# Kernel tuning notes

Hardware: AMD Instinct MI355X
Metric: run time of the kernel (lower is better)

Reference implementation:

```python
import jax, jax.numpy as jnp
import numpy as np

B, N, D, H = 128, 512, 128, 8
DK = D // H
CLIP = 10.0                      # tanh_clipping
NORM = float(np.sqrt(D))         # norm_factor = sqrt(embedding_dim), used as multiplier (as in source)


def setup_inputs() -> dict:
    key = jax.random.key(0)
    ks = jax.random.split(key, 7)
    std = float(1.0 / np.sqrt(D))
    return {
        "embeddings": jax.random.normal(ks[0], (B, N, D), dtype=jnp.float32),
        "eval_seq": jax.random.randint(ks[1], (B, N), 0, N, dtype=jnp.int32),
        "W_placeholder": jax.random.uniform(ks[2], (2 * D,), jnp.float32, -std, std),
        "W_node": jax.random.normal(ks[3], (D, 3 * D), jnp.float32) * std,
        "W_fixed": jax.random.normal(ks[4], (D, D), jnp.float32) * std,
        "W_step": jax.random.normal(ks[5], (2 * D, D), jnp.float32) * std,
        "W_out": jax.random.normal(ks[6], (D, D), jnp.float32) * std,
    }


def _decode(embeddings, eval_seq, W_placeholder, W_node, W_fixed, W_step, W_out):
    # Precomputed (fixed) projections, as in the torch module before the decode loop
    proj = embeddings @ W_node                                  # [B,N,3D]
    gK, gV, lK = jnp.split(proj, 3, axis=-1)
    gK = gK.reshape(B, N, H, DK).transpose(2, 0, 1, 3)          # [H,B,N,dk]
    gV = gV.reshape(B, N, H, DK).transpose(2, 0, 1, 3)          # [H,B,N,dk]
    fixed = embeddings.mean(axis=1) @ W_fixed                   # [B,D]
    batch_ix = jnp.arange(B)

    def step_logp(ctx, mask):
        # ctx: [B,2D] step context; mask: [B,N] bool (True = visited)
        query = fixed + ctx @ W_step                            # [B,D]
        qh = query.reshape(B, H, DK)
        compat = NORM * jnp.einsum('bhd,hbnd->hbn', qh, gK)     # [H,B,N]
        compat = jnp.where(mask[None], -jnp.inf, compat)        # mask_inner
        attn = jax.nn.softmax(compat, axis=-1)
        heads = jnp.einsum('hbn,hbnd->hbd', attn, gV)           # [H,B,dk]
        glimpse = heads.transpose(1, 0, 2).reshape(B, D) @ W_out
        logits = NORM * jnp.einsum('bnd,bd->bn', lK, glimpse)   # [B,N]
        logits = jnp.tanh(logits) * CLIP
        logits = jnp.where(mask, -jnp.inf, logits)              # mask_logits
        return jax.nn.log_softmax(logits, axis=-1)              # temp = 1.0

    # step 0: W_placeholder context, empty mask
    mask0 = jnp.zeros((B, N), dtype=bool)
    ctx0 = jnp.broadcast_to(W_placeholder[None, :], (B, 2 * D))
    lp0 = step_logp(ctx0, mask0)
    sel0 = eval_seq[:, 0]
    mask1 = mask0.at[batch_ix, sel0].set(True)
    emb_first = embeddings[batch_ix, sel0]                      # [B,D] (constant across steps)

    def body(carry, sel_i):
        mask, last = carry
        ctx = jnp.concatenate([emb_first, embeddings[batch_ix, last]], axis=-1)  # [B,2D]
        lp = step_logp(ctx, mask)
        new_mask = mask.at[batch_ix, sel_i].set(True)           # update mask AFTER computing log_p
        return (new_mask, sel_i), lp

    (_, _), lps = jax.lax.scan(body, (mask1, sel0), eval_seq[:, 1:].T)  # lps: [N-1,B,N]
    log_p = jnp.concatenate([lp0[None], lps], axis=0).transpose(1, 0, 2)  # [B,N,N]
    return log_p


def reference(embeddings, eval_seq, W_placeholder, W_node, W_fixed, W_step, W_out):
    log_p = _decode(embeddings, eval_seq, W_placeholder, W_node, W_fixed, W_step, W_out)
    return log_p, eval_seq
```

## Files before the change

### kernel.cpp

```cpp
#include <hip/hip_runtime.h>
#include <math.h>

#define B_ 128
#define N_ 512
#define D_ 128
#define H_ 8
#define NORM_ 11.313708498984761f
#define SC_ 16.322324f
#define HSC_ 32.644648f
#define CLIP_ 10.0f
#define MASKC_ -3.0e38f
#define NEG_BIG_ -1.0e30f
#define L2E_ 1.4426950408889634f
#define LN2_ 0.6931471805599453f

typedef unsigned short ushortx;
typedef __attribute__((ext_vector_type(8))) short s8v;
typedef __attribute__((ext_vector_type(4))) float f4v;

#define MFMA_ __builtin_amdgcn_mfma_f32_16x16x32_bf16

__device__ __forceinline__ unsigned short f2bf(float x) {
  union { float f; unsigned u; } v; v.f = x;
  unsigned r = v.u + 0x7fffu + ((v.u >> 16) & 1u);
  return (unsigned short)(r >> 16);
}
__device__ __forceinline__ float bf2f(ushortx u) {
  union { unsigned u; float f; } v; v.u = ((unsigned)u) << 16; return v.f;
}
__device__ __forceinline__ unsigned cvtpk(float lo, float hi) {
  unsigned r;
  asm("v_cvt_pk_bf16_f32 %0, %1, %2" : "=v"(r) : "v"(lo), "v"(hi));
  return r;
}
__device__ __forceinline__ float exp2_hw(float x) {
  float r; asm("v_exp_f32 %0, %1" : "=v"(r) : "v"(x)); return r;
}
__device__ __forceinline__ float log2_hw(float x) {
  float r; asm("v_log_f32 %0, %1" : "=v"(r) : "v"(x)); return r;
}
__device__ __forceinline__ float rcp_hw(float x) {
  float r; asm("v_rcp_f32 %0, %1" : "=v"(r) : "v"(x)); return r;
}
__device__ __forceinline__ float max3f(float a, float b, float c) {
  float r; asm("v_max3_f32 %0, %1, %2, %3" : "=v"(r) : "v"(a), "v"(b), "v"(c));
  return r;
}

__global__ __launch_bounds__(128)
void wfold2(const float* __restrict__ Wnode, const float* __restrict__ Wout,
            const float* __restrict__ Wstep, ushortx* __restrict__ WfT,
            ushortx* __restrict__ WsbT) {
  const int c = blockIdx.x;
  const int k = threadIdx.x;
  if (c < 256) {
    WfT[c * 128 + k] = f2bf(Wnode[k * 384 + c]);
  } else if (c < 384) {
    const int d = c - 256;
    float s = 0.f;
    #pragma unroll 4
    for (int j = 0; j < 128; ++j) s += Wnode[k * 384 + 256 + j] * Wout[d * 128 + j];
    WfT[c * 128 + k] = f2bf(s);
  } else {
    const int d = c - 384;
    WsbT[d * 128 + k] = f2bf(Wstep[(128 + k) * 128 + d] * SC_);
  }
}

__global__ void t_init(int* __restrict__ T) {
  T[blockIdx.x * 256 + threadIdx.x] = 0x7fffffff;
}
__global__ void t_scatter(const int* __restrict__ seq, int* __restrict__ T) {
  const int i = blockIdx.x * 256 + threadIdx.x;
  const int b = i >> 9, st = i & 511;
  atomicMin(&T[b * N_ + seq[i]], st + 1);
}

__global__ __launch_bounds__(512)
void sortperm(const int* __restrict__ seq, const int* __restrict__ T,
              ushortx* __restrict__ K, ushortx* __restrict__ n_orig) {
  const int b = blockIdx.x;
  const int t = threadIdx.x;
  const int lane = t & 63, wv = t >> 6;
  __shared__ int wsum[8];
  __shared__ int tot_s;

  const int node = seq[b * 512 + t];
  const int f = (T[b * 512 + node] == t + 1) ? 1 : 0;
  const unsigned long long bal = __ballot(f);
  const int excl = __popcll(bal & ((1ull << lane) - 1ull));
  if (lane == 0) wsum[wv] = __popcll(bal);
  __syncthreads();
  int woff = 0;
  #pragma unroll
  for (int i = 0; i < 8; ++i) woff += (i < wv) ? wsum[i] : 0;
  const int Kt = woff + excl;
  K[b * 512 + t] = (ushortx)Kt;
  if (f) n_orig[b * 512 + Kt] = (ushortx)node;
  if (t == 511) tot_s = Kt + f;

  const int g = (T[b * 512 + t] == 0x7fffffff) ? 1 : 0;
  const unsigned long long bal2 = __ballot(g);
  const int excl2 = __popcll(bal2 & ((1ull << lane) - 1ull));
  const int w2 = __popcll(bal2);
  __syncthreads();
  if (lane == 0) wsum[wv] = w2;
  __syncthreads();
  int woff2 = 0;
  #pragma unroll
  for (int i = 0; i < 8; ++i) woff2 += (i < wv) ? wsum[i] : 0;
  if (g) n_orig[b * 512 + tot_s + woff2 + excl2] = (ushortx)t;
}

__global__ __launch_bounds__(256)
void proj_mfma(const float* __restrict__ E, const ushortx* __restrict__ WfT,
               const ushortx* __restrict__ n_orig,
               ushortx* __restrict__ gK, ushortx* __restrict__ gVt,
               ushortx* __restrict__ lKt) {
  __shared__ ushortx S[64 * 216];
  const int tid = threadIdx.x;
  const int w = tid >> 6, l = tid & 63;
  const int m16 = l & 15, lg = l >> 4;
  const int b = blockIdx.x >> 3;
  const int n0 = (blockIdx.x & 7) * 64;
  const int p_row = n0 + w * 16 + m16;
  const int orig = (int)n_orig[b * 512 + p_row];
  const float* er = E + ((size_t)b * 512 + orig) * 128;

  s8v af[4];
  #pragma unroll
  for (int ks = 0; ks < 4; ++ks) {
    float4 f0 = *(const float4*)(er + ks * 32 + lg * 8);
    float4 f1 = *(const float4*)(er + ks * 32 + lg * 8 + 4);
    union { unsigned u[4]; s8v v; } au;
    au.u[0] = cvtpk(f0.x, f0.y); au.u[1] = cvtpk(f0.z, f0.w);
    au.u[2] = cvtpk(f1.x, f1.y); au.u[3] = cvtpk(f1.z, f1.w);
    af[ks] = au.v;
  }

  const int lrow = w * 16 + 4 * lg;
  #pragma unroll
  for (int half = 0; half < 2; ++half) {
    const int cb = half * 192;
    #pragma unroll
    for (int ct = 0; ct < 12; ++ct) {
      const int lc = ct * 16 + m16;
      f4v acc = {0.f, 0.f, 0.f, 0.f};
      #pragma unroll
      for (int ks = 0; ks < 4; ++ks) {
        const s8v bf = *(const s8v*)(WfT + (size_t)(cb + lc) * 128 + ks * 32 + lg * 8);
        acc = MFMA_(af[ks], bf, acc, 0, 0, 0);
      }
      const unsigned w01 = cvtpk(acc[0], acc[1]);
      const unsigned w23 = cvtpk(acc[2], acc[3]);
      S[(lrow + 0) * 216 + lc] = (ushortx)(w01 & 0xffffu);
      S[(lrow + 1) * 216 + lc] = (ushortx)(w01 >> 16);
      S[(lrow + 2) * 216 + lc] = (ushortx)(w23 & 0xffffu);
      S[(lrow + 3) * 216 + lc] = (ushortx)(w23 >> 16);
    }
    __syncthreads();

    if (half == 0) {
      #pragma unroll
      for (int it = 0; it < 4; ++it) {
        const int idx = it * 256 + tid;
        const int hh = idx >> 7, nn = (idx >> 1) & 63, hf = idx & 1;
        const uint4 v = *(const uint4*)(&S[nn * 216 + hh * 16 + hf * 8]);
        *(uint4*)(gK + (((size_t)(b * 8 + hh) * 512 + n0 + nn) * 16 + hf * 8)) = v;
      }
      #pragma unroll
      for (int it = 0; it < 2; ++it) {
        const int idx = it * 256 + tid;
        const int hh = idx >> 7, dk = (idx >> 3) & 15, n8 = (idx & 7) * 8;
        const int lc = 128 + hh * 16 + dk;
        unsigned wr[4];
        #pragma unroll
        for (int j = 0; j < 4; ++j)
          wr[j] = (unsigned)S[(n8 + 2 * j) * 216 + lc] |
                  ((unsigned)S[(n8 + 2 * j + 1) * 216 + lc] << 16);
        uint4 o; o.x = wr[0]; o.y = wr[1]; o.z = wr[2]; o.w = wr[3];
        *(uint4*)(gVt + (((size_t)(b * 8 + hh) * 16 + dk) * 512 + n0 + n8)) = o;
      }
    } else {
      #pragma unroll
      for (int it = 0; it < 4; ++it) {
        const int idx = it * 256 + tid;
        const int nn = idx >> 4, d8 = (idx & 15) * 8;
        const uint4 v = *(const uint4*)(&S[nn * 216 + 64 + d8]);
        *(uint4*)(lKt + ((size_t)(b * 512 + n0 + nn) * 128 + d8)) = v;
      }
      #pragma unroll
      for (int it = 0; it < 2; ++it) {
        const int idx = it * 256 + tid;
        const int hq = idx >> 7, dk = (idx >> 3) & 15, n8 = (idx & 7) * 8;
        const int lc = hq * 16 + dk;
        unsigned wr[4];
        #pragma unroll
        for (int j = 0; j < 4; ++j)
          wr[j] = (unsigned)S[(n8 + 2 * j) * 216 + lc] |
                  ((unsigned)S[(n8 + 2 * j + 1) * 216 + lc] << 16);
        uint4 o; o.x = wr[0]; o.y = wr[1]; o.z = wr[2]; o.w = wr[3];
        *(uint4*)(gVt + (((size_t)(b * 8 + 4 + hq) * 16 + dk) * 512 + n0 + n8)) = o;
      }
    }
    __syncthreads();
  }
}

__global__ __launch_bounds__(512)
void prep(const float* __restrict__ emb, const int* __restrict__ seq,
          const float* __restrict__ Wp, const float* __restrict__ Wfix,
          const float* __restrict__ Wstep, ushortx* __restrict__ Qb,
          float* __restrict__ Abuf) {
  const int b = blockIdx.x;
  const int t = threadIdx.x;
  const int q = t >> 7, d = t & 127;
  __shared__ float red[4][128];
  __shared__ float mean[128];
  const float* eb = emb + (size_t)b * N_ * D_;
  float sum = 0.f;
  for (int n = q; n < 512; n += 4) sum += eb[(size_t)n * 128 + d];
  red[q][d] = sum;
  __syncthreads();
  if (t < 128) mean[t] = (red[0][t] + red[1][t] + red[2][t] + red[3][t]) * (1.f / 512.f);
  __syncthreads();
  if (t < 128) {
    float fx = 0.f;
    for (int k = 0; k < 128; ++k) fx += mean[k] * Wfix[k * 128 + t];
    float c = 0.f;
    for (int k = 0; k < 256; ++k) c += Wp[k] * Wstep[k * 128 + t];
    const int sel0 = seq[b * N_];
    const float* ef = eb + (size_t)sel0 * 128;
    float a = 0.f;
    for (int k = 0; k < 128; ++k) a += ef[k] * Wstep[k * 128 + t];
    Qb[b * 128 + t] = f2bf((fx + c) * SC_);
    Abuf[b * 128 + t] = (fx + a) * SC_;
  }
}

__global__ __launch_bounds__(256)
void qstep_mfma(const float* __restrict__ emb, const int* __restrict__ seq,
                const ushortx* __restrict__ WsbT, const float* __restrict__ Abuf,
                ushortx* __restrict__ Qb) {
  const int sg = blockIdx.x, b = blockIdx.y;
  const int tid = threadIdx.x;
  const int w = tid >> 6, l = tid & 63;
  const int m16 = l & 15, lg = l >> 4;
  __shared__ int sel_l[128];
  __shared__ float Ab[128];
  if (tid < 128) {
    const int s = sg * 128 + tid;
    sel_l[tid] = (s >= 1) ? seq[b * N_ + s - 1] : 0;
    Ab[tid] = Abuf[b * 128 + tid];
  }
  __syncthreads();

  #pragma unroll
  for (int ts = 0; ts < 2; ++ts) {
    const int srow = (w * 2 + ts) * 16;
    const int gr = sel_l[srow + m16];
    const float* er = emb + ((size_t)b * 512 + gr) * 128;
    s8v af[4];
    #pragma unroll
    for (int ks = 0; ks < 4; ++ks) {
      float4 f0 = *(const float4*)(er + ks * 32 + lg * 8);
      float4 f1 = *(const float4*)(er + ks * 32 + lg * 8 + 4);
      union { unsigned u[4]; s8v v; } au;
      au.u[0] = cvtpk(f0.x, f0.y); au.u[1] = cvtpk(f0.z, f0.w);
      au.u[2] = cvtpk(f1.x, f1.y); au.u[3] = cvtpk(f1.z, f1.w);
      af[ks] = au.v;
    }
    #pragma unroll
    for (int dt = 0; dt < 8; ++dt) {
      const int col = dt * 16 + m16;
      f4v acc = {0.f, 0.f, 0.f, 0.f};
      #pragma unroll
      for (int ks = 0; ks < 4; ++ks) {
        const s8v bf = *(const s8v*)(WsbT + (size_t)col * 128 + ks * 32 + lg * 8);
        acc = MFMA_(af[ks], bf, acc, 0, 0, 0);
      }
      const float ab = Ab[col];
      #pragma unroll
      for (int r = 0; r < 4; ++r) {
        const int s = sg * 128 + srow + 4 * lg + r;
        if (s > 0) Qb[((size_t)s * B_ + b) * D_ + col] = f2bf(acc[r] + ab);
      }
    }
  }
}

__global__ void tail_seq(const int* __restrict__ seq, float* __restrict__ out,
                         int count) {
  const int i = blockIdx.x * 256 + threadIdx.x;
  if (i < count) out[(size_t)B_ * N_ * N_ + i] = (float)seq[i];
}

__global__ __launch_bounds__(512, 8)
void decode_mfma(const ushortx* __restrict__ gK,
                 const ushortx* __restrict__ gVt,
                 const ushortx* __restrict__ lKt,
                 const ushortx* __restrict__ Qb,
                 const ushortx* __restrict__ Ksrt,
                 const ushortx* __restrict__ n_orig,
                 float* __restrict__ out) {
  const int id = blockIdx.x;
  const int xcd = id & 7, pos = id >> 3;
  const int b = xcd * 16 + (pos >> 5);
  const int s0 = (pos & 31) * 16;
  const int tid = threadIdx.x;
  const int w = tid >> 6;
  const int l = tid & 63;
  const int m16 = l & 15;
  const int lg = l >> 4;

  __shared__ ushortx logitsTb[512 * 26];
  __shared__ ushortx heads_lds[16][136];
  __shared__ ushortx norig_l[512];
  __shared__ ushortx Ko[16];

  norig_l[tid] = n_orig[b * 512 + tid];
  if (tid < 16) Ko[tid] = Ksrt[b * 512 + s0 + tid];
  __syncthreads();

  const int h = w;
  const int Ks = (int)Ko[m16];
  const int K0i = (int)Ko[0];
  const int K15i = (int)Ko[15];
  const int chStart = K0i >> 5;
  const int chClean = (K15i + 31) >> 5;
  const size_t bh512 = (size_t)(b * 8 + h) * 512;

  s8v qf = {};
  if (lg < 2)
    qf = *reinterpret_cast<const s8v*>(
        Qb + (((size_t)(s0 + m16) * B_ + b) * D_ + h * 16 + lg * 8));

  f4v Oacc = {0.f, 0.f, 0.f, 0.f};
  float m_run = NEG_BIG_, l_run = 0.f;
  const int nA0 = 8 * (m16 >> 2) + (m16 & 3);

  for (int ch = chStart; ch < 16; ++ch) {
    const int base = ch * 32;
    s8v a0 = {}, a1 = {};
    if (lg < 2) {
      a0 = *reinterpret_cast<const s8v*>(gK + ((bh512 + base + nA0) * 16 + lg * 8));
      a1 = *reinterpret_cast<const s8v*>(gK + ((bh512 + base + nA0 + 4) * 16 + lg * 8));
    }
    const s8v av = *reinterpret_cast<const s8v*>(
        gVt + (((bh512 * 16) >> 9) * 512 + (size_t)m16 * 512 + base + lg * 8));

    f4v z = {0.f, 0.f, 0.f, 0.f};
    f4v st0 = MFMA_(a0, qf, z, 0, 0, 0);
    f4v st1 = MFMA_(a1, qf, z, 0, 0, 0);

    float cm = max3f(st0[0], st0[1], st0[2]);
    cm = max3f(cm, st0[3], st1[0]);
    cm = max3f(cm, st1[1], st1[2]);
    cm = fmaxf(cm, st1[3]);
    cm = fmaxf(cm, __shfl_xor(cm, 16));
    cm = fmaxf(cm, __shfl_xor(cm, 32));

    if (__any(cm > m_run + 8.0f)) {
      const float mnew = fmaxf(m_run, cm);
      const float corr = exp2_hw(m_run - mnew);
      m_run = mnew;
      l_run *= corr;
      Oacc[0] *= corr; Oacc[1] *= corr; Oacc[2] *= corr; Oacc[3] *= corr;
    }

    float p[8];
    #pragma unroll
    for (int r = 0; r < 4; ++r) {
      p[r]     = exp2_hw(st0[r] - m_run);
      p[4 + r] = exp2_hw(st1[r] - m_run);
    }
    if (ch < chClean) {
      const int nb = base + 8 * lg;
      #pragma unroll
      for (int j = 0; j < 8; ++j) p[j] = (nb + j < Ks) ? 0.f : p[j];
    }
    l_run += ((p[0] + p[1]) + (p[2] + p[3])) + ((p[4] + p[5]) + (p[6] + p[7]));
    union { unsigned u[4]; s8v v; } pu;
    pu.u[0] = cvtpk(p[0], p[1]); pu.u[1] = cvtpk(p[2], p[3]);
    pu.u[2] = cvtpk(p[4], p[5]); pu.u[3] = cvtpk(p[6], p[7]);
    Oacc = MFMA_(av, pu.v, Oacc, 0, 0, 0);
  }

  l_run += __shfl_xor(l_run, 16);
  l_run += __shfl_xor(l_run, 32);
  const float scale = rcp_hw(l_run) * HSC_;
  #pragma unroll
  for (int r = 0; r < 4; ++r)
    heads_lds[m16][h * 16 + 4 * lg + r] = f2bf(Oacc[r] * scale);
  __syncthreads();

  #pragma unroll
  for (int nt = 0; nt < 4; ++nt) {
    const int n0 = w * 64 + nt * 16;
    if (n0 + 16 <= K0i) {
      #pragma unroll
      for (int r = 0; r < 4; ++r)
        logitsTb[(n0 + 4 * lg + r) * 26 + m16] = f2bf(MASKC_);
      continue;
    }
    f4v acc = {0.f, 0.f, 0.f, 0.f};
    #pragma unroll
    for (int ks = 0; ks < 4; ++ks) {
      const s8v aL = *reinterpret_cast<const s8v*>(
          lKt + (((size_t)b * 512 + n0 + m16) * 128 + ks * 32 + lg * 8));
      const s8v bH = *reinterpret_cast<const s8v*>(&heads_lds[m16][ks * 32 + lg * 8]);
      acc = MFMA_(aL, bH, acc, 0, 0, 0);
    }
    const bool bnd = (n0 < K15i);
    #pragma unroll
    for (int r = 0; r < 4; ++r) {
      const int n = n0 + 4 * lg + r;
      float x = fminf(fmaxf(acc[r], -43.f), 43.f);
      const float e2 = exp2_hw(x);
      float lgv = CLIP_ * (e2 - 1.f) * rcp_hw(e2 + 1.f);
      if (bnd && n < Ks) lgv = MASKC_;
      logitsTb[n * 26 + m16] = f2bf(lgv);
    }
  }
  __syncthreads();

  int no[8];
  #pragma unroll
  for (int i = 0; i < 8; ++i) no[i] = (int)norig_l[i * 64 + l];
  #pragma unroll
  for (int pass = 0; pass < 2; ++pass) {
    const int s = w + pass * 8;
    float v[8];
    #pragma unroll
    for (int i = 0; i < 8; ++i) v[i] = bf2f(logitsTb[(i * 64 + l) * 26 + s]);
    float mm = max3f(v[0], v[1], v[2]);
    mm = max3f(mm, v[3], v[4]);
    mm = max3f(mm, v[5], v[6]);
    mm = fmaxf(mm, v[7]);
    #pragma unroll
    for (int off = 1; off <= 32; off <<= 1) mm = fmaxf(mm, __shfl_xor(mm, off));
    float es = 0.f;
    #pragma unroll
    for (int i = 0; i < 8; ++i) es += exp2_hw((v[i] - mm) * L2E_);
    #pragma unroll
    for (int off = 1; off <= 32; off <<= 1) es += __shfl_xor(es, off);
    const float logZ = mm + LN2_ * log2_hw(es);
    float* orow = out + ((size_t)(b * N_ + s0 + s)) * N_;
    #pragma unroll
    for (int i = 0; i < 8; ++i)
      orow[no[i]] = fmaxf(v[i] - logZ, NEG_BIG_);
  }
}

extern "C" void kernel_launch(void* const* d_in, const int* in_sizes, int n_in,
                              void* d_out, int out_size, void* d_ws, size_t ws_size,
                              hipStream_t stream) {
  const float* emb   = (const float*)d_in[0];
  const int*   seq   = (const int*)d_in[1];
  const float* Wp    = (const float*)d_in[2];
  const float* Wnode = (const float*)d_in[3];
  const float* Wfix  = (const float*)d_in[4];
  const float* Wstep = (const float*)d_in[5];
  const float* Wout  = (const float*)d_in[6];
  float* out = (float*)d_out;

  ushortx* gK    = (ushortx*)d_ws;
  ushortx* gVt   = gK   + (size_t)8388608;
  ushortx* lKt   = gVt  + (size_t)8388608;
  ushortx* Qb    = lKt  + (size_t)8388608;
  ushortx* WfT   = Qb   + (size_t)8388608;
  ushortx* WsbT  = WfT  + (size_t)49152;
  ushortx* Ksrt  = WsbT + (size_t)16384;
  ushortx* n_or  = Ksrt + (size_t)65536;
  float*   Abuf  = (float*)(n_or + (size_t)65536);
  int*     T     = (int*)(Abuf + 16384);

  wfold2<<<512, 128, 0, stream>>>(Wnode, Wout, Wstep, WfT, WsbT);
  t_init<<<256, 256, 0, stream>>>(T);
  t_scatter<<<256, 256, 0, stream>>>(seq, T);
  sortperm<<<128, 512, 0, stream>>>(seq, T, Ksrt, n_or);
  proj_mfma<<<1024, 256, 0, stream>>>(emb, WfT, n_or, gK, gVt, lKt);
  prep<<<128, 512, 0, stream>>>(emb, seq, Wp, Wfix, Wstep, Qb, Abuf);
  qstep_mfma<<<dim3(4, 128), 256, 0, stream>>>(emb, seq, WsbT, Abuf, Qb);
  decode_mfma<<<4096, 512, 0, stream>>>(gK, gVt, lKt, Qb, Ksrt, n_or, out);

  const long long lp_elems = (long long)B_ * N_ * N_;
  const int tail = (int)((long long)out_size - lp_elems);
  if (tail > 0) {
    tail_seq<<<(tail + 255) / 256, 256, 0, stream>>>(seq, out, tail);
  }
}
```

Before: 277.9 us.

## Fuse query projection into decode kernel and process 32 steps per block

Removes the separate qstep_mfma kernel and its global Qb buffer by computing each step's query inside decode_mfma from gathered embeddings and WsbT. Each block now handles 32 decode steps instead of 16, so gK/gVt/lKt loads are shared by two query tiles, halving the grid. The final log-softmax keeps logits in registers and reduces across waves through small LDS arrays instead of a transposed bf16 LDS buffer. The prep mean reduction is also vectorized with float4 loads. This raises register pressure in the decode kernel and may reduce occupancy.

Measured after the change: 280.7 us. Within noise of the previous version (+1.0%).

```diff
diff --git a/kernel.cpp b/kernel.cpp
--- a/kernel.cpp
+++ b/kernel.cpp
@@ -24,9 +24,6 @@
   union { float f; unsigned u; } v; v.f = x;
   unsigned r = v.u + 0x7fffu + ((v.u >> 16) & 1u);
   return (unsigned short)(r >> 16);
-}
-__device__ __forceinline__ float bf2f(ushortx u) {
-  union { unsigned u; float f; } v; v.u = ((unsigned)u) << 16; return v.f;
 }
 __device__ __forceinline__ unsigned cvtpk(float lo, float hi) {
   unsigned r;
@@ -210,19 +207,28 @@
 __global__ __launch_bounds__(512)
 void prep(const float* __restrict__ emb, const int* __restrict__ seq,
           const float* __restrict__ Wp, const float* __restrict__ Wfix,
-          const float* __restrict__ Wstep, ushortx* __restrict__ Qb,
+          const float* __restrict__ Wstep, ushortx* __restrict__ Qb0,
           float* __restrict__ Abuf) {
   const int b = blockIdx.x;
   const int t = threadIdx.x;
-  const int q = t >> 7, d = t & 127;
-  __shared__ float red[4][128];
+  __shared__ float4 red4[16][33];
   __shared__ float mean[128];
-  const float* eb = emb + (size_t)b * N_ * D_;
-  float sum = 0.f;
-  for (int n = q; n < 512; n += 4) sum += eb[(size_t)n * 128 + d];
-  red[q][d] = sum;
-  __syncthreads();
-  if (t < 128) mean[t] = (red[0][t] + red[1][t] + red[2][t] + red[3][t]) * (1.f / 512.f);
+  const int row0 = t >> 5, c4 = t & 31;
+  const float* eb = emb + (size_t)b * 512 * 128;
+  float4 acc = {0.f, 0.f, 0.f, 0.f};
+  for (int it = 0; it < 32; ++it) {
+    const float4 x = *(const float4*)(eb + (size_t)(it * 16 + row0) * 128 + c4 * 4);
+    acc.x += x.x; acc.y += x.y; acc.z += x.z; acc.w += x.w;
+  }
+  red4[row0][c4] = acc;
+  __syncthreads();
+  if (t < 128) {
+    const int c4b = t >> 2, j = t & 3;
+    float s = 0.f;
+    #pragma unroll
+    for (int r = 0; r < 16; ++r) s += ((const float*)&red4[r][c4b])[j];
+    mean[t] = s * (1.f / 512.f);
+  }
   __syncthreads();
   if (t < 128) {
     float fx = 0.f;
@@ -233,59 +239,8 @@
     const float* ef = eb + (size_t)sel0 * 128;
     float a = 0.f;
     for (int k = 0; k < 128; ++k) a += ef[k] * Wstep[k * 128 + t];
-    Qb[b * 128 + t] = f2bf((fx + c) * SC_);
+    Qb0[b * 128 + t] = f2bf((fx + c) * SC_);
     Abuf[b * 128 + t] = (fx + a) * SC_;
-  }
-}
-
-__global__ __launch_bounds__(256)
-void qstep_mfma(const float* __restrict__ emb, const int* __restrict__ seq,
-                const ushortx* __restrict__ WsbT, const float* __restrict__ Abuf,
-                ushortx* __restrict__ Qb) {
-  const int sg = blockIdx.x, b = blockIdx.y;
-  const int tid = threadIdx.x;
-  const int w = tid >> 6, l = tid & 63;
-  const int m16 = l & 15, lg = l >> 4;
-  __shared__ int sel_l[128];
-  __shared__ float Ab[128];
-  if (tid < 128) {
-    const int s = sg * 128 + tid;
-    sel_l[tid] = (s >= 1) ? seq[b * N_ + s - 1] : 0;
-    Ab[tid] = Abuf[b * 128 + tid];
-  }
-  __syncthreads();
-
-  #pragma unroll
-  for (int ts = 0; ts < 2; ++ts) {
-    const int srow = (w * 2 + ts) * 16;
-    const int gr = sel_l[srow + m16];
-    const float* er = emb + ((size_t)b * 512 + gr) * 128;
-    s8v af[4];
-    #pragma unroll
-    for (int ks = 0; ks < 4; ++ks) {
-      float4 f0 = *(const float4*)(er + ks * 32 + lg * 8);
-      float4 f1 = *(const float4*)(er + ks * 32 + lg * 8 + 4);
-      union { unsigned u[4]; s8v v; } au;
-      au.u[0] = cvtpk(f0.x, f0.y); au.u[1] = cvtpk(f0.z, f0.w);
-      au.u[2] = cvtpk(f1.x, f1.y); au.u[3] = cvtpk(f1.z, f1.w);
-      af[ks] = au.v;
-    }
-    #pragma unroll
-    for (int dt = 0; dt < 8; ++dt) {
-      const int col = dt * 16 + m16;
-      f4v acc = {0.f, 0.f, 0.f, 0.f};
-      #pragma unroll
-      for (int ks = 0; ks < 4; ++ks) {
-        const s8v bf = *(const s8v*)(WsbT + (size_t)col * 128 + ks * 32 + lg * 8);
-        acc = MFMA_(af[ks], bf, acc, 0, 0, 0);
-      }
-      const float ab = Ab[col];
-      #pragma unroll
-      for (int r = 0; r < 4; ++r) {
-        const int s = sg * 128 + srow + 4 * lg + r;
-        if (s > 0) Qb[((size_t)s * B_ + b) * D_ + col] = f2bf(acc[r] + ab);
-      }
-    }
   }
 }
 
@@ -299,156 +254,279 @@
 void decode_mfma(const ushortx* __restrict__ gK,
                  const ushortx* __restrict__ gVt,
                  const ushortx* __restrict__ lKt,
-                 const ushortx* __restrict__ Qb,
+                 const float* __restrict__ emb,
+                 const int* __restrict__ seq,
+                 const ushortx* __restrict__ WsbT,
+                 const float* __restrict__ Abuf,
+                 const ushortx* __restrict__ Qb0,
                  const ushortx* __restrict__ Ksrt,
                  const ushortx* __restrict__ n_orig,
                  float* __restrict__ out) {
   const int id = blockIdx.x;
   const int xcd = id & 7, pos = id >> 3;
-  const int b = xcd * 16 + (pos >> 5);
-  const int s0 = (pos & 31) * 16;
+  const int b = xcd * 16 + (pos >> 4);
+  const int s0 = (pos & 15) * 32;
   const int tid = threadIdx.x;
-  const int w = tid >> 6;
-  const int l = tid & 63;
-  const int m16 = l & 15;
-  const int lg = l >> 4;
-
-  __shared__ ushortx logitsTb[512 * 26];
-  __shared__ ushortx heads_lds[16][136];
+  const int w = tid >> 6, l = tid & 63;
+  const int m16 = l & 15, lg = l >> 4;
+
   __shared__ ushortx norig_l[512];
-  __shared__ ushortx Ko[16];
+  __shared__ ushortx Ko[32];
+  __shared__ int sel_l[32];
+  __shared__ float Ab[128];
+  __shared__ ushortx ctxh[32][136];
+  __shared__ ushortx Qt[32][136];
+  __shared__ float red1[8][32];
+  __shared__ float red2[8][32];
 
   norig_l[tid] = n_orig[b * 512 + tid];
-  if (tid < 16) Ko[tid] = Ksrt[b * 512 + s0 + tid];
+  if (tid < 32) {
+    Ko[tid] = Ksrt[b * 512 + s0 + tid];
+    const int sg = s0 + tid;
+    sel_l[tid] = (sg >= 1) ? seq[b * 512 + sg - 1] : 0;
+  }
+  if (tid < 128) Ab[tid] = Abuf[b * 128 + tid];
+  __syncthreads();
+
+  {
+    const int row = tid >> 4, c8 = (tid & 15) * 8;
+    const float* er = emb + ((size_t)b * 512 + sel_l[row]) * 128 + c8;
+    float4 f0 = *(const float4*)(er);
+    float4 f1 = *(const float4*)(er + 4);
+    unsigned* dst = (unsigned*)&ctxh[row][c8];
+    dst[0] = cvtpk(f0.x, f0.y); dst[1] = cvtpk(f0.z, f0.w);
+    dst[2] = cvtpk(f1.x, f1.y); dst[3] = cvtpk(f1.z, f1.w);
+  }
   __syncthreads();
 
   const int h = w;
-  const int Ks = (int)Ko[m16];
-  const int K0i = (int)Ko[0];
-  const int K15i = (int)Ko[15];
+  {
+    s8v aw[4];
+    #pragma unroll
+    for (int ks = 0; ks < 4; ++ks)
+      aw[ks] = *(const s8v*)(WsbT + (size_t)(h * 16 + m16) * 128 + ks * 32 + lg * 8);
+    #pragma unroll
+    for (int t = 0; t < 2; ++t) {
+      f4v acc = {0.f, 0.f, 0.f, 0.f};
+      #pragma unroll
+      for (int ks = 0; ks < 4; ++ks) {
+        const s8v bf = *(const s8v*)(&ctxh[t * 16 + m16][ks * 32 + lg * 8]);
+        acc = MFMA_(aw[ks], bf, acc, 0, 0, 0);
+      }
+      const int d0 = h * 16 + 4 * lg;
+      unsigned q01 = cvtpk(acc[0] + Ab[d0], acc[1] + Ab[d0 + 1]);
+      unsigned q23 = cvtpk(acc[2] + Ab[d0 + 2], acc[3] + Ab[d0 + 3]);
+      if (s0 == 0 && t == 0 && m16 == 0) {
+        q01 = *(const unsigned*)(Qb0 + b * 128 + d0);
+        q23 = *(const unsigned*)(Qb0 + b * 128 + d0 + 2);
+      }
+      unsigned* qdst = (unsigned*)&Qt[t * 16 + m16][d0];
+      qdst[0] = q01; qdst[1] = q23;
+    }
+  }
+  __syncthreads();
+
+  s8v qfA = {}, qfB = {};
+  if (lg < 2) {
+    qfA = *(const s8v*)(&Qt[m16][h * 16 + lg * 8]);
+    qfB = *(const s8v*)(&Qt[16 + m16][h * 16 + lg * 8]);
+  }
+
+  const int K0i = (int)Ko[0], K15 = (int)Ko[15], K31 = (int)Ko[31];
   const int chStart = K0i >> 5;
-  const int chClean = (K15i + 31) >> 5;
-  const size_t bh512 = (size_t)(b * 8 + h) * 512;
-
-  s8v qf = {};
-  if (lg < 2)
-    qf = *reinterpret_cast<const s8v*>(
-        Qb + (((size_t)(s0 + m16) * B_ + b) * D_ + h * 16 + lg * 8));
-
-  f4v Oacc = {0.f, 0.f, 0.f, 0.f};
-  float m_run = NEG_BIG_, l_run = 0.f;
+  const int chCleanA = (K15 + 31) >> 5;
+  const int chCleanB = (K31 + 31) >> 5;
+  const int KsA = (int)Ko[m16], KsB = (int)Ko[16 + m16];
+  const size_t bh = (size_t)(b * 8 + h);
+
+  f4v OA = {0.f,0.f,0.f,0.f}, OB = {0.f,0.f,0.f,0.f};
+  float mA = NEG_BIG_, mB = NEG_BIG_, lA = 0.f, lB = 0.f;
   const int nA0 = 8 * (m16 >> 2) + (m16 & 3);
 
   for (int ch = chStart; ch < 16; ++ch) {
     const int base = ch * 32;
     s8v a0 = {}, a1 = {};
     if (lg < 2) {
-      a0 = *reinterpret_cast<const s8v*>(gK + ((bh512 + base + nA0) * 16 + lg * 8));
-      a1 = *reinterpret_cast<const s8v*>(gK + ((bh512 + base + nA0 + 4) * 16 + lg * 8));
-    }
-    const s8v av = *reinterpret_cast<const s8v*>(
-        gVt + (((bh512 * 16) >> 9) * 512 + (size_t)m16 * 512 + base + lg * 8));
-
-    f4v z = {0.f, 0.f, 0.f, 0.f};
-    f4v st0 = MFMA_(a0, qf, z, 0, 0, 0);
-    f4v st1 = MFMA_(a1, qf, z, 0, 0, 0);
-
-    float cm = max3f(st0[0], st0[1], st0[2]);
-    cm = max3f(cm, st0[3], st1[0]);
-    cm = max3f(cm, st1[1], st1[2]);
-    cm = fmaxf(cm, st1[3]);
-    cm = fmaxf(cm, __shfl_xor(cm, 16));
-    cm = fmaxf(cm, __shfl_xor(cm, 32));
-
-    if (__any(cm > m_run + 8.0f)) {
-      const float mnew = fmaxf(m_run, cm);
-      const float corr = exp2_hw(m_run - mnew);
-      m_run = mnew;
-      l_run *= corr;
-      Oacc[0] *= corr; Oacc[1] *= corr; Oacc[2] *= corr; Oacc[3] *= corr;
-    }
-
-    float p[8];
-    #pragma unroll
-    for (int r = 0; r < 4; ++r) {
-      p[r]     = exp2_hw(st0[r] - m_run);
-      p[4 + r] = exp2_hw(st1[r] - m_run);
-    }
-    if (ch < chClean) {
-      const int nb = base + 8 * lg;
-      #pragma unroll
-      for (int j = 0; j < 8; ++j) p[j] = (nb + j < Ks) ? 0.f : p[j];
-    }
-    l_run += ((p[0] + p[1]) + (p[2] + p[3])) + ((p[4] + p[5]) + (p[6] + p[7]));
-    union { unsigned u[4]; s8v v; } pu;
-    pu.u[0] = cvtpk(p[0], p[1]); pu.u[1] = cvtpk(p[2], p[3]);
-    pu.u[2] = cvtpk(p[4], p[5]); pu.u[3] = cvtpk(p[6], p[7]);
-    Oacc = MFMA_(av, pu.v, Oacc, 0, 0, 0);
-  }
-
-  l_run += __shfl_xor(l_run, 16);
-  l_run += __shfl_xor(l_run, 32);
-  const float scale = rcp_hw(l_run) * HSC_;
-  #pragma unroll
-  for (int r = 0; r < 4; ++r)
-    heads_lds[m16][h * 16 + 4 * lg + r] = f2bf(Oacc[r] * scale);
-  __syncthreads();
-
+      a0 = *(const s8v*)(gK + ((bh * 512 + base + nA0) * 16 + lg * 8));
+      a1 = *(const s8v*)(gK + ((bh * 512 + base + nA0 + 4) * 16 + lg * 8));
+    }
+    const s8v av = *(const s8v*)(gVt + ((bh * 16 + m16) * 512 + base + lg * 8));
+    const int nb = base + 8 * lg;
+
+    {
+      f4v z = {0.f,0.f,0.f,0.f};
+      f4v st0 = MFMA_(a0, qfA, z, 0, 0, 0);
+      f4v st1 = MFMA_(a1, qfA, z, 0, 0, 0);
+      float cm = max3f(st0[0], st0[1], st0[2]);
+      cm = max3f(cm, st0[3], st1[0]);
+      cm = max3f(cm, st1[1], st1[2]);
+      cm = fmaxf(cm, st1[3]);
+      cm = fmaxf(cm, __shfl_xor(cm, 16));
+      cm = fmaxf(cm, __shfl_xor(cm, 32));
+      if (__any(cm > mA + 8.f)) {
+        const float mn = fmaxf(mA, cm);
+        const float cr = exp2_hw(mA - mn);
+        mA = mn; lA *= cr;
+        OA[0] *= cr; OA[1] *= cr; OA[2] *= cr; OA[3] *= cr;
+      }
+      float p[8];
+      #pragma unroll
+      for (int r = 0; r < 4; ++r) {
+        p[r] = exp2_hw(st0[r] - mA);
+        p[4 + r] = exp2_hw(st1[r] - mA);
+      }
+      if (ch < chCleanA) {
+        #pragma unroll
+        for (int j = 0; j < 8; ++j) p[j] = (nb + j < KsA) ? 0.f : p[j];
+      }
+      lA += ((p[0]+p[1])+(p[2]+p[3])) + ((p[4]+p[5])+(p[6]+p[7]));
+      union { unsigned u[4]; s8v v; } pu;
+      pu.u[0] = cvtpk(p[0], p[1]); pu.u[1] = cvtpk(p[2], p[3]);
+      pu.u[2] = cvtpk(p[4], p[5]); pu.u[3] = cvtpk(p[6], p[7]);
+      OA = MFMA_(av, pu.v, OA, 0, 0, 0);
+    }
+    {
+      f4v z = {0.f,0.f,0.f,0.f};
+      f4v st0 = MFMA_(a0, qfB, z, 0, 0, 0);
+      f4v st1 = MFMA_(a1, qfB, z, 0, 0, 0);
+      float cm = max3f(st0[0], st0[1], st0[2]);
+      cm = max3f(cm, st0[3], st1[0]);
+      cm = max3f(cm, st1[1], st1[2]);
+      cm = fmaxf(cm, st1[3]);
+      cm = fmaxf(cm, __shfl_xor(cm, 16));
+      cm = fmaxf(cm, __shfl_xor(cm, 32));
+      if (__any(cm > mB + 8.f)) {
+        const float mn = fmaxf(mB, cm);
+        const float cr = exp2_hw(mB - mn);
+        mB = mn; lB *= cr;
+        OB[0] *= cr; OB[1] *= cr; OB[2] *= cr; OB[3] *= cr;
+      }
+      float p[8];
+      #pragma unroll
+      for (int r = 0; r < 4; ++r) {
+        p[r] = exp2_hw(st0[r] - mB);
+        p[4 + r] = exp2_hw(st1[r] - mB);
+      }
+      if (ch < chCleanB) {
+        #pragma unroll
+        for (int j = 0; j < 8; ++j) p[j] = (nb + j < KsB) ? 0.f : p[j];
+      }
+      lB += ((p[0]+p[1])+(p[2]+p[3])) + ((p[4]+p[5])+(p[6]+p[7]));
+      union { unsigned u[4]; s8v v; } pu;
+      pu.u[0] = cvtpk(p[0], p[1]); pu.u[1] = cvtpk(p[2], p[3]);
+      pu.u[2] = cvtpk(p[4], p[5]); pu.u[3] = cvtpk(p[6], p[7]);
+      OB = MFMA_(av, pu.v, OB, 0, 0, 0);
+    }
+  }
+
+  lA += __shfl_xor(lA, 16); lA += __shfl_xor(lA, 32);
+  lB += __shfl_xor(lB, 16); lB += __shfl_xor(lB, 32);
+  const float scA = rcp_hw(lA) * HSC_;
+  const float scB = rcp_hw(lB) * HSC_;
+  {
+    const int d0 = h * 16 + 4 * lg;
+    unsigned* hd = (unsigned*)&ctxh[m16][d0];
+    hd[0] = cvtpk(OA[0] * scA, OA[1] * scA);
+    hd[1] = cvtpk(OA[2] * scA, OA[3] * scA);
+    unsigned* hd2 = (unsigned*)&ctxh[16 + m16][d0];
+    hd2[0] = cvtpk(OB[0] * scB, OB[1] * scB);
+    hd2[1] = cvtpk(OB[2] * scB, OB[3] * scB);
+  }
+  __syncthreads();
+
+  float v[4][8];
   #pragma unroll
   for (int nt = 0; nt < 4; ++nt) {
     const int n0 = w * 64 + nt * 16;
     if (n0 + 16 <= K0i) {
       #pragma unroll
-      for (int r = 0; r < 4; ++r)
-        logitsTb[(n0 + 4 * lg + r) * 26 + m16] = f2bf(MASKC_);
+      for (int j = 0; j < 8; ++j) v[nt][j] = MASKC_;
       continue;
     }
-    f4v acc = {0.f, 0.f, 0.f, 0.f};
+    f4v accA = {0.f,0.f,0.f,0.f}, accB = {0.f,0.f,0.f,0.f};
     #pragma unroll
     for (int ks = 0; ks < 4; ++ks) {
-      const s8v aL = *reinterpret_cast<const s8v*>(
-          lKt + (((size_t)b * 512 + n0 + m16) * 128 + ks * 32 + lg * 8));
-      const s8v bH = *reinterpret_cast<const s8v*>(&heads_lds[m16][ks * 32 + lg * 8]);
-      acc = MFMA_(aL, bH, acc, 0, 0, 0);
-    }
-    const bool bnd = (n0 < K15i);
+      const s8v aL = *(const s8v*)(lKt + ((size_t)b * 512 + n0 + m16) * 128 + ks * 32 + lg * 8);
+      const s8v hA = *(const s8v*)(&ctxh[m16][ks * 32 + lg * 8]);
+      const s8v hB = *(const s8v*)(&ctxh[16 + m16][ks * 32 + lg * 8]);
+      accA = MFMA_(aL, hA, accA, 0, 0, 0);
+      accB = MFMA_(aL, hB, accB, 0, 0, 0);
+    }
+    const bool bndA = (n0 < K15), bndB = (n0 < K31);
     #pragma unroll
     for (int r = 0; r < 4; ++r) {
-      const int n = n0 + 4 * lg + r;
-      float x = fminf(fmaxf(acc[r], -43.f), 43.f);
-      const float e2 = exp2_hw(x);
-      float lgv = CLIP_ * (e2 - 1.f) * rcp_hw(e2 + 1.f);
-      if (bnd && n < Ks) lgv = MASKC_;
-      logitsTb[n * 26 + m16] = f2bf(lgv);
-    }
-  }
-  __syncthreads();
-
-  int no[8];
-  #pragma unroll
-  for (int i = 0; i < 8; ++i) no[i] = (int)norig_l[i * 64 + l];
-  #pragma unroll
-  for (int pass = 0; pass < 2; ++pass) {
-    const int s = w + pass * 8;
-    float v[8];
-    #pragma unroll
-    for (int i = 0; i < 8; ++i) v[i] = bf2f(logitsTb[(i * 64 + l) * 26 + s]);
-    float mm = max3f(v[0], v[1], v[2]);
-    mm = max3f(mm, v[3], v[4]);
-    mm = max3f(mm, v[5], v[6]);
-    mm = fmaxf(mm, v[7]);
-    #pragma unroll
-    for (int off = 1; off <= 32; off <<= 1) mm = fmaxf(mm, __shfl_xor(mm, off));
-    float es = 0.f;
-    #pragma unroll
-    for (int i = 0; i < 8; ++i) es += exp2_hw((v[i] - mm) * L2E_);
-    #pragma unroll
-    for (int off = 1; off <= 32; off <<= 1) es += __shfl_xor(es, off);
-    const float logZ = mm + LN2_ * log2_hw(es);
-    float* orow = out + ((size_t)(b * N_ + s0 + s)) * N_;
-    #pragma unroll
-    for (int i = 0; i < 8; ++i)
-      orow[no[i]] = fmaxf(v[i] - logZ, NEG_BIG_);
+      const int p = n0 + 4 * lg + r;
+      float xA = fminf(fmaxf(accA[r], -43.f), 43.f);
+      const float eA = exp2_hw(xA);
+      float vA = CLIP_ * (eA - 1.f) * rcp_hw(eA + 1.f);
+      if (bndA && p < KsA) vA = MASKC_;
+      v[nt][r] = vA;
+      float xB = fminf(fmaxf(accB[r], -43.f), 43.f);
+      const float eB = exp2_hw(xB);
+      float vB = CLIP_ * (eB - 1.f) * rcp_hw(eB + 1.f);
+      if (bndB && p < KsB) vB = MASKC_;
+      v[nt][4 + r] = vB;
+    }
+  }
+
+  float wmA = max3f(v[0][0], v[0][1], v[0][2]);
+  wmA = max3f(wmA, v[0][3], v[1][0]);
+  wmA = max3f(wmA, v[1][1], v[1][2]);
+  wmA = max3f(wmA, v[1][3], v[2][0]);
+  wmA = max3f(wmA, v[2][1], v[2][2]);
+  wmA = max3f(wmA, v[2][3], v[3][0]);
+  wmA = max3f(wmA, v[3][1], v[3][2]);
+  wmA = fmaxf(wmA, v[3][3]);
+  float wmB = max3f(v[0][4], v[0][5], v[0][6]);
+  wmB = max3f(wmB, v[0][7], v[1][4]);
+  wmB = max3f(wmB, v[1][5], v[1][6]);
+  wmB = max3f(wmB, v[1][7], v[2][4]);
+  wmB = max3f(wmB, v[2][5], v[2][6]);
+  wmB = max3f(wmB, v[2][7], v[3][4]);
+  wmB = max3f(wmB, v[3][5], v[3][6]);
+  wmB = fmaxf(wmB, v[3][7]);
+  wmA = fmaxf(wmA, __shfl_xor(wmA, 16)); wmA = fmaxf(wmA, __shfl_xor(wmA, 32));
+  wmB = fmaxf(wmB, __shfl_xor(wmB, 16)); wmB = fmaxf(wmB, __shfl_xor(wmB, 32));
+  if (l < 16) red1[w][m16] = wmA;
+  else if (l < 32) red1[w][16 + m16] = wmB;
+  __syncthreads();
+  float MA = red1[0][m16], MB = red1[0][16 + m16];
+  #pragma unroll
+  for (int k = 1; k < 8; ++k) {
+    MA = fmaxf(MA, red1[k][m16]);
+    MB = fmaxf(MB, red1[k][16 + m16]);
+  }
+  float esA = 0.f, esB = 0.f;
+  #pragma unroll
+  for (int nt = 0; nt < 4; ++nt) {
+    #pragma unroll
+    for (int r = 0; r < 4; ++r) {
+      esA += exp2_hw((v[nt][r] - MA) * L2E_);
+      esB += exp2_hw((v[nt][4 + r] - MB) * L2E_);
+    }
+  }
+  esA += __shfl_xor(esA, 16); esA += __shfl_xor(esA, 32);
+  esB += __shfl_xor(esB, 16); esB += __shfl_xor(esB, 32);
+  if (l < 16) red2[w][m16] = esA;
+  else if (l < 32) red2[w][16 + m16] = esB;
+  __syncthreads();
+  float sA = 0.f, sB = 0.f;
+  #pragma unroll
+  for (int k = 0; k < 8; ++k) { sA += red2[k][m16]; sB += red2[k][16 + m16]; }
+  const float lzA = MA + LN2_ * log2_hw(sA);
+  const float lzB = MB + LN2_ * log2_hw(sB);
+
+  float* orowA = out + ((size_t)(b * 512 + s0 + m16)) * 512;
+  float* orowB = out + ((size_t)(b * 512 + s0 + 16 + m16)) * 512;
+  #pragma unroll
+  for (int nt = 0; nt < 4; ++nt) {
+    #pragma unroll
+    for (int r = 0; r < 4; ++r) {
+      const int p = w * 64 + nt * 16 + 4 * lg + r;
+      const int no = (int)norig_l[p];
+      orowA[no] = fmaxf(v[nt][r] - lzA, NEG_BIG_);
+      orowB[no] = fmaxf(v[nt][4 + r] - lzB, NEG_BIG_);
+    }
   }
 }
 
@@ -467,12 +545,12 @@
   ushortx* gK    = (ushortx*)d_ws;
   ushortx* gVt   = gK   + (size_t)8388608;
   ushortx* lKt   = gVt  + (size_t)8388608;
-  ushortx* Qb    = lKt  + (size_t)8388608;
-  ushortx* WfT   = Qb   + (size_t)8388608;
+  ushortx* WfT   = lKt  + (size_t)8388608;
   ushortx* WsbT  = WfT  + (size_t)49152;
   ushortx* Ksrt  = WsbT + (size_t)16384;
   ushortx* n_or  = Ksrt + (size_t)65536;
-  float*   Abuf  = (float*)(n_or + (size_t)65536);
+  ushortx* Qb0   = n_or + (size_t)65536;
+  float*   Abuf  = (float*)(Qb0 + (size_t)16384);
   int*     T     = (int*)(Abuf + 16384);
 
   wfold2<<<512, 128, 0, stream>>>(Wnode, Wout, Wstep, WfT, WsbT);
@@ -480,9 +558,9 @@
   t_scatter<<<256, 256, 0, stream>>>(seq, T);
   sortperm<<<128, 512, 0, stream>>>(seq, T, Ksrt, n_or);
   proj_mfma<<<1024, 256, 0, stream>>>(emb, WfT, n_or, gK, gVt, lKt);
-  prep<<<128, 512, 0, stream>>>(emb, seq, Wp, Wfix, Wstep, Qb, Abuf);
-  qstep_mfma<<<dim3(4, 128), 256, 0, stream>>>(emb, seq, WsbT, Abuf, Qb);
-  decode_mfma<<<4096, 512, 0, stream>>>(gK, gVt, lKt, Qb, Ksrt, n_or, out);
+  prep<<<128, 512, 0, stream>>>(emb, seq, Wp, Wfix, Wstep, Qb0, Abuf);
+  decode_mfma<<<2048, 512, 0, stream>>>(gK, gVt, lKt, emb, seq, WsbT, Abuf,
+                                        Qb0, Ksrt, n_or, out);
 
   const long long lp_elems = (long long)B_ * N_ * N_;
   const int tail = (int)((long long)out_size - lp_elems);
```

## Fuse query projection into decode and move first-visit table into LDS

Applied to the files above, without the earlier changes.

Removes the separate qstep kernel and its 16 MB Qb intermediate. Each decode block now gathers its 16 previous-node embeddings, converts them to bf16 in LDS and computes its query tile with MFMA before attention. The t_init and t_scatter kernels are folded into sortperm through an LDS atomicMin table, and prep's mean reduction is vectorized with float4 loads. This saves launches and global traffic, at the cost of extra LDS and a small amount of redundant-free work added to the start of each decode block.

Result: faster. 241.1 us (median of 2 runs) (-13.2%).

```diff
diff --git a/kernel.cpp b/kernel.cpp
--- a/kernel.cpp
+++ b/kernel.cpp
@@ -67,26 +67,23 @@
   }
 }
 
-__global__ void t_init(int* __restrict__ T) {
-  T[blockIdx.x * 256 + threadIdx.x] = 0x7fffffff;
-}
-__global__ void t_scatter(const int* __restrict__ seq, int* __restrict__ T) {
-  const int i = blockIdx.x * 256 + threadIdx.x;
-  const int b = i >> 9, st = i & 511;
-  atomicMin(&T[b * N_ + seq[i]], st + 1);
-}
-
 __global__ __launch_bounds__(512)
-void sortperm(const int* __restrict__ seq, const int* __restrict__ T,
-              ushortx* __restrict__ K, ushortx* __restrict__ n_orig) {
+void sortperm(const int* __restrict__ seq, ushortx* __restrict__ K,
+              ushortx* __restrict__ n_orig) {
   const int b = blockIdx.x;
   const int t = threadIdx.x;
   const int lane = t & 63, wv = t >> 6;
+  __shared__ int Tl[512];
   __shared__ int wsum[8];
   __shared__ int tot_s;
 
+  Tl[t] = 0x7fffffff;
+  __syncthreads();
   const int node = seq[b * 512 + t];
-  const int f = (T[b * 512 + node] == t + 1) ? 1 : 0;
+  atomicMin(&Tl[node], t + 1);
+  __syncthreads();
+
+  const int f = (Tl[node] == t + 1) ? 1 : 0;
   const unsigned long long bal = __ballot(f);
   const int excl = __popcll(bal & ((1ull << lane) - 1ull));
   if (lane == 0) wsum[wv] = __popcll(bal);
@@ -99,7 +96,7 @@
   if (f) n_orig[b * 512 + Kt] = (ushortx)node;
   if (t == 511) tot_s = Kt + f;
 
-  const int g = (T[b * 512 + t] == 0x7fffffff) ? 1 : 0;
+  const int g = (Tl[t] == 0x7fffffff) ? 1 : 0;
   const unsigned long long bal2 = __ballot(g);
   const int excl2 = __popcll(bal2 & ((1ull << lane) - 1ull));
   const int w2 = __popcll(bal2);
@@ -210,19 +207,28 @@
 __global__ __launch_bounds__(512)
 void prep(const float* __restrict__ emb, const int* __restrict__ seq,
           const float* __restrict__ Wp, const float* __restrict__ Wfix,
-          const float* __restrict__ Wstep, ushortx* __restrict__ Qb,
+          const float* __restrict__ Wstep, ushortx* __restrict__ Qb0,
           float* __restrict__ Abuf) {
   const int b = blockIdx.x;
   const int t = threadIdx.x;
-  const int q = t >> 7, d = t & 127;
-  __shared__ float red[4][128];
+  __shared__ float4 red4[16][33];
   __shared__ float mean[128];
-  const float* eb = emb + (size_t)b * N_ * D_;
-  float sum = 0.f;
-  for (int n = q; n < 512; n += 4) sum += eb[(size_t)n * 128 + d];
-  red[q][d] = sum;
-  __syncthreads();
-  if (t < 128) mean[t] = (red[0][t] + red[1][t] + red[2][t] + red[3][t]) * (1.f / 512.f);
+  const int row0 = t >> 5, c4 = t & 31;
+  const float* eb = emb + (size_t)b * 512 * 128;
+  float4 acc = {0.f, 0.f, 0.f, 0.f};
+  for (int it = 0; it < 32; ++it) {
+    const float4 x = *(const float4*)(eb + (size_t)(it * 16 + row0) * 128 + c4 * 4);
+    acc.x += x.x; acc.y += x.y; acc.z += x.z; acc.w += x.w;
+  }
+  red4[row0][c4] = acc;
+  __syncthreads();
+  if (t < 128) {
+    const int c4b = t >> 2, j = t & 3;
+    float s = 0.f;
+    #pragma unroll
+    for (int r = 0; r < 16; ++r) s += ((const float*)&red4[r][c4b])[j];
+    mean[t] = s * (1.f / 512.f);
+  }
   __syncthreads();
   if (t < 128) {
     float fx = 0.f;
@@ -233,59 +239,8 @@
     const float* ef = eb + (size_t)sel0 * 128;
     float a = 0.f;
     for (int k = 0; k < 128; ++k) a += ef[k] * Wstep[k * 128 + t];
-    Qb[b * 128 + t] = f2bf((fx + c) * SC_);
+    Qb0[b * 128 + t] = f2bf((fx + c) * SC_);
     Abuf[b * 128 + t] = (fx + a) * SC_;
-  }
-}
-
-__global__ __launch_bounds__(256)
-void qstep_mfma(const float* __restrict__ emb, const int* __restrict__ seq,
-                const ushortx* __restrict__ WsbT, const float* __restrict__ Abuf,
-                ushortx* __restrict__ Qb) {
-  const int sg = blockIdx.x, b = blockIdx.y;
-  const int tid = threadIdx.x;
-  const int w = tid >> 6, l = tid & 63;
-  const int m16 = l & 15, lg = l >> 4;
-  __shared__ int sel_l[128];
-  __shared__ float Ab[128];
-  if (tid < 128) {
-    const int s = sg * 128 + tid;
-    sel_l[tid] = (s >= 1) ? seq[b * N_ + s - 1] : 0;
-    Ab[tid] = Abuf[b * 128 + tid];
-  }
-  __syncthreads();
-
-  #pragma unroll
-  for (int ts = 0; ts < 2; ++ts) {
-    const int srow = (w * 2 + ts) * 16;
-    const int gr = sel_l[srow + m16];
-    const float* er = emb + ((size_t)b * 512 + gr) * 128;
-    s8v af[4];
-    #pragma unroll
-    for (int ks = 0; ks < 4; ++ks) {
-      float4 f0 = *(const float4*)(er + ks * 32 + lg * 8);
-      float4 f1 = *(const float4*)(er + ks * 32 + lg * 8 + 4);
-      union { unsigned u[4]; s8v v; } au;
-      au.u[0] = cvtpk(f0.x, f0.y); au.u[1] = cvtpk(f0.z, f0.w);
-      au.u[2] = cvtpk(f1.x, f1.y); au.u[3] = cvtpk(f1.z, f1.w);
-      af[ks] = au.v;
-    }
-    #pragma unroll
-    for (int dt = 0; dt < 8; ++dt) {
-      const int col = dt * 16 + m16;
-      f4v acc = {0.f, 0.f, 0.f, 0.f};
-      #pragma unroll
-      for (int ks = 0; ks < 4; ++ks) {
-        const s8v bf = *(const s8v*)(WsbT + (size_t)col * 128 + ks * 32 + lg * 8);
-        acc = MFMA_(af[ks], bf, acc, 0, 0, 0);
-      }
-      const float ab = Ab[col];
-      #pragma unroll
-      for (int r = 0; r < 4; ++r) {
-        const int s = sg * 128 + srow + 4 * lg + r;
-        if (s > 0) Qb[((size_t)s * B_ + b) * D_ + col] = f2bf(acc[r] + ab);
-      }
-    }
   }
 }
 
@@ -299,7 +254,11 @@
 void decode_mfma(const ushortx* __restrict__ gK,
                  const ushortx* __restrict__ gVt,
                  const ushortx* __restrict__ lKt,
-                 const ushortx* __restrict__ Qb,
+                 const float* __restrict__ emb,
+                 const int* __restrict__ seq,
+                 const ushortx* __restrict__ WsbT,
+                 const float* __restrict__ Abuf,
+                 const ushortx* __restrict__ Qb0,
                  const ushortx* __restrict__ Ksrt,
                  const ushortx* __restrict__ n_orig,
                  float* __restrict__ out) {
@@ -308,32 +267,69 @@
   const int b = xcd * 16 + (pos >> 5);
   const int s0 = (pos & 31) * 16;
   const int tid = threadIdx.x;
-  const int w = tid >> 6;
-  const int l = tid & 63;
-  const int m16 = l & 15;
-  const int lg = l >> 4;
+  const int w = tid >> 6, l = tid & 63;
+  const int m16 = l & 15, lg = l >> 4;
 
   __shared__ ushortx logitsTb[512 * 26];
-  __shared__ ushortx heads_lds[16][136];
+  __shared__ ushortx ctxh[16][136];
+  __shared__ ushortx Qt[16][136];
   __shared__ ushortx norig_l[512];
   __shared__ ushortx Ko[16];
+  __shared__ int sel_l[16];
+  __shared__ float Ab[128];
 
   norig_l[tid] = n_orig[b * 512 + tid];
-  if (tid < 16) Ko[tid] = Ksrt[b * 512 + s0 + tid];
+  if (tid < 16) {
+    Ko[tid] = Ksrt[b * 512 + s0 + tid];
+    const int sg = s0 + tid;
+    sel_l[tid] = (sg >= 1) ? seq[b * 512 + sg - 1] : 0;
+  }
+  if (tid < 128) Ab[tid] = Abuf[b * 128 + tid];
+  __syncthreads();
+
+  if (tid < 256) {
+    const int row = tid >> 4, c8 = (tid & 15) * 8;
+    const float* er = emb + ((size_t)b * 512 + sel_l[row]) * 128 + c8;
+    float4 f0 = *(const float4*)(er);
+    float4 f1 = *(const float4*)(er + 4);
+    unsigned* dst = (unsigned*)&ctxh[row][c8];
+    dst[0] = cvtpk(f0.x, f0.y); dst[1] = cvtpk(f0.z, f0.w);
+    dst[2] = cvtpk(f1.x, f1.y); dst[3] = cvtpk(f1.z, f1.w);
+  }
   __syncthreads();
 
   const int h = w;
+  {
+    s8v aw[4];
+    #pragma unroll
+    for (int ks = 0; ks < 4; ++ks)
+      aw[ks] = *(const s8v*)(WsbT + (size_t)(h * 16 + m16) * 128 + ks * 32 + lg * 8);
+    f4v acc = {0.f, 0.f, 0.f, 0.f};
+    #pragma unroll
+    for (int ks = 0; ks < 4; ++ks) {
+      const s8v bf = *(const s8v*)(&ctxh[m16][ks * 32 + lg * 8]);
+      acc = MFMA_(aw[ks], bf, acc, 0, 0, 0);
+    }
+    const int d0 = h * 16 + 4 * lg;
+    unsigned q01 = cvtpk(acc[0] + Ab[d0], acc[1] + Ab[d0 + 1]);
+    unsigned q23 = cvtpk(acc[2] + Ab[d0 + 2], acc[3] + Ab[d0 + 3]);
+    if (s0 == 0 && m16 == 0) {
+      q01 = *(const unsigned*)(Qb0 + b * 128 + d0);
+      q23 = *(const unsigned*)(Qb0 + b * 128 + d0 + 2);
+    }
+    unsigned* qdst = (unsigned*)&Qt[m16][d0];
+    qdst[0] = q01; qdst[1] = q23;
+  }
+  __syncthreads();
+
+  s8v qf = {};
+  if (lg < 2) qf = *(const s8v*)(&Qt[m16][h * 16 + lg * 8]);
+
+  const int K0i = (int)Ko[0], K15 = (int)Ko[15];
+  const int chStart = K0i >> 5;
+  const int chClean = (K15 + 31) >> 5;
   const int Ks = (int)Ko[m16];
-  const int K0i = (int)Ko[0];
-  const int K15i = (int)Ko[15];
-  const int chStart = K0i >> 5;
-  const int chClean = (K15i + 31) >> 5;
-  const size_t bh512 = (size_t)(b * 8 + h) * 512;
-
-  s8v qf = {};
-  if (lg < 2)
-    qf = *reinterpret_cast<const s8v*>(
-        Qb + (((size_t)(s0 + m16) * B_ + b) * D_ + h * 16 + lg * 8));
+  const size_t bh = (size_t)(b * 8 + h);
 
   f4v Oacc = {0.f, 0.f, 0.f, 0.f};
   float m_run = NEG_BIG_, l_run = 0.f;
@@ -343,11 +339,10 @@
     const int base = ch * 32;
     s8v a0 = {}, a1 = {};
     if (lg < 2) {
-      a0 = *reinterpret_cast<const s8v*>(gK + ((bh512 + base + nA0) * 16 + lg * 8));
-      a1 = *reinterpret_cast<const s8v*>(gK + ((bh512 + base + nA0 + 4) * 16 + lg * 8));
-    }
-    const s8v av = *reinterpret_cast<const s8v*>(
-        gVt + (((bh512 * 16) >> 9) * 512 + (size_t)m16 * 512 + base + lg * 8));
+      a0 = *(const s8v*)(gK + ((bh * 512 + base + nA0) * 16 + lg * 8));
+      a1 = *(const s8v*)(gK + ((bh * 512 + base + nA0 + 4) * 16 + lg * 8));
+    }
+    const s8v av = *(const s8v*)(gVt + ((bh * 16 + m16) * 512 + base + lg * 8));
 
     f4v z = {0.f, 0.f, 0.f, 0.f};
     f4v st0 = MFMA_(a0, qf, z, 0, 0, 0);
@@ -361,11 +356,10 @@
     cm = fmaxf(cm, __shfl_xor(cm, 32));
 
     if (__any(cm > m_run + 8.0f)) {
-      const float mnew = fmaxf(m_run, cm);
-      const float corr = exp2_hw(m_run - mnew);
-      m_run = mnew;
-      l_run *= corr;
-      Oacc[0] *= corr; Oacc[1] *= corr; Oacc[2] *= corr; Oacc[3] *= corr;
+      const float mn = fmaxf(m_run, cm);
+      const float cr = exp2_hw(m_run - mn);
+      m_run = mn; l_run *= cr;
+      Oacc[0] *= cr; Oacc[1] *= cr; Oacc[2] *= cr; Oacc[3] *= cr;
     }
 
     float p[8];
@@ -389,9 +383,12 @@
   l_run += __shfl_xor(l_run, 16);
   l_run += __shfl_xor(l_run, 32);
   const float scale = rcp_hw(l_run) * HSC_;
-  #pragma unroll
-  for (int r = 0; r < 4; ++r)
-    heads_lds[m16][h * 16 + 4 * lg + r] = f2bf(Oacc[r] * scale);
+  {
+    const int d0 = h * 16 + 4 * lg;
+    unsigned* hd = (unsigned*)&ctxh[m16][d0];
+    hd[0] = cvtpk(Oacc[0] * scale, Oacc[1] * scale);
+    hd[1] = cvtpk(Oacc[2] * scale, Oacc[3] * scale);
+  }
   __syncthreads();
 
   #pragma unroll
@@ -406,20 +403,19 @@
     f4v acc = {0.f, 0.f, 0.f, 0.f};
     #pragma unroll
     for (int ks = 0; ks < 4; ++ks) {
-      const s8v aL = *reinterpret_cast<const s8v*>(
-          lKt + (((size_t)b * 512 + n0 + m16) * 128 + ks * 32 + lg * 8));
-      const s8v bH = *reinterpret_cast<const s8v*>(&heads_lds[m16][ks * 32 + lg * 8]);
+      const s8v aL = *(const s8v*)(lKt + ((size_t)b * 512 + n0 + m16) * 128 + ks * 32 + lg * 8);
+      const s8v bH = *(const s8v*)(&ctxh[m16][ks * 32 + lg * 8]);
       acc = MFMA_(aL, bH, acc, 0, 0, 0);
     }
-    const bool bnd = (n0 < K15i);
+    const bool bnd = (n0 < K15);
     #pragma unroll
     for (int r = 0; r < 4; ++r) {
-      const int n = n0 + 4 * lg + r;
+      const int p = n0 + 4 * lg + r;
       float x = fminf(fmaxf(acc[r], -43.f), 43.f);
       const float e2 = exp2_hw(x);
       float lgv = CLIP_ * (e2 - 1.f) * rcp_hw(e2 + 1.f);
-      if (bnd && n < Ks) lgv = MASKC_;
-      logitsTb[n * 26 + m16] = f2bf(lgv);
+      if (bnd && p < Ks) lgv = MASKC_;
+      logitsTb[p * 26 + m16] = f2bf(lgv);
     }
   }
   __syncthreads();
@@ -467,22 +463,19 @@
   ushortx* gK    = (ushortx*)d_ws;
   ushortx* gVt   = gK   + (size_t)8388608;
   ushortx* lKt   = gVt  + (size_t)8388608;
-  ushortx* Qb    = lKt  + (size_t)8388608;
-  ushortx* WfT   = Qb   + (size_t)8388608;
+  ushortx* WfT   = lKt  + (size_t)8388608;
   ushortx* WsbT  = WfT  + (size_t)49152;
   ushortx* Ksrt  = WsbT + (size_t)16384;
   ushortx* n_or  = Ksrt + (size_t)65536;
-  float*   Abuf  = (float*)(n_or + (size_t)65536);
-  int*     T     = (int*)(Abuf + 16384);
+  ushortx* Qb0   = n_or + (size_t)65536;
+  float*   Abuf  = (float*)(Qb0 + (size_t)16384);
 
   wfold2<<<512, 128, 0, stream>>>(Wnode, Wout, Wstep, WfT, WsbT);
-  t_init<<<256, 256, 0, stream>>>(T);
-  t_scatter<<<256, 256, 0, stream>>>(seq, T);
-  sortperm<<<128, 512, 0, stream>>>(seq, T, Ksrt, n_or);
+  sortperm<<<128, 512, 0, stream>>>(seq, Ksrt, n_or);
   proj_mfma<<<1024, 256, 0, stream>>>(emb, WfT, n_or, gK, gVt, lKt);
-  prep<<<128, 512, 0, stream>>>(emb, seq, Wp, Wfix, Wstep, Qb, Abuf);
-  qstep_mfma<<<dim3(4, 128), 256, 0, stream>>>(emb, seq, WsbT, Abuf, Qb);
-  decode_mfma<<<4096, 512, 0, stream>>>(gK, gVt, lKt, Qb, Ksrt, n_or, out);
+  prep<<<128, 512, 0, stream>>>(emb, seq, Wp, Wfix, Wstep, Qb0, Abuf);
+  decode_mfma<<<4096, 512, 0, stream>>>(gK, gVt, lKt, emb, seq, WsbT, Abuf,
+                                        Qb0, Ksrt, n_or, out);
 
   const long long lp_elems = (long long)B_ * N_ * N_;
   const int tail = (int)((long long)out_size - lp_elems);
```
